# Kernel tuning notes

Hardware: AMD Instinct MI355X
Metric: run time of the kernel (lower is better)

## Reference

```python
import jax, jax.numpy as jnp
import numpy as np

DEPTH = 9
NUM_LEAVES = 2 ** DEPTH            # 512
NUM_BRANCHES = 2 ** DEPTH - 1      # 511


def _leaf_paths(depth):
    """For each leaf, the BFS (heap-order) branch indices along its root->leaf
    path and the left/right bit taken at each branch (1 = right)."""
    L = 2 ** depth
    idx = np.zeros((L, depth), np.int32)
    bits = np.zeros((L, depth), np.int32)
    for l in range(L):
        node = 0
        for t in range(depth):
            b = (l >> (depth - 1 - t)) & 1
            idx[l, t] = node
            bits[l, t] = b
            node = 2 * node + 1 + b
    return jnp.asarray(idx), jnp.asarray(bits)

PATH_IDX, PATH_BITS = _leaf_paths(DEPTH)


def setup_inputs() -> dict:
    key = jax.random.key(0)
    k1, k2, k3 = jax.random.split(key, 3)
    B, D, W, H = 128, 256, 28, 28
    C = 200
    return {
        "xs": jax.random.normal(k1, (B, D, W, H), jnp.float32),
        "prototypes": jax.random.normal(k2, (NUM_BRANCHES, D, 1, 1), jnp.float32),
        "leaf_params": jax.random.normal(k3, (NUM_LEAVES, C), jnp.float32),
    }


def reference(xs, prototypes, leaf_params):
    # ---- L2Conv2D: squared-L2 distance map via conv decomposition ----
    B, D, W, H = xs.shape
    P = prototypes.shape[0]
    p = prototypes.reshape(P, D)                       # W1 = H1 = 1
    x2 = jnp.sum(xs * xs, axis=1)                      # [B, W, H]
    p2 = jnp.sum(p * p, axis=1)                        # [P]
    xp = jnp.einsum('bdwh,pd->bpwh', xs, p)            # [B, P, W, H]
    sq = x2[:, None] - 2.0 * xp + p2[None, :, None, None]
    distances = jnp.sqrt(jnp.abs(sq) + 1e-14)          # [B, P, W, H]

    # ---- min-pool over full spatial extent (avg-pool unused: focal off) ----
    min_distances = jnp.min(distances, axis=(2, 3))    # [B, P]
    similarities = jnp.exp(-min_distances)             # [B, P], ps per branch

    # ---- soft tree routing: pa(leaf) = prod over path of ps / (1-ps) ----
    ps_path = similarities[:, PATH_IDX]                # [B, L, depth]
    step = jnp.where(PATH_BITS[None] == 1, ps_path, 1.0 - ps_path)
    pa = jnp.prod(step, axis=-1)                       # [B, L]

    # ---- mix leaf class distributions (distributed sampling strategy) ----
    ds = jax.nn.softmax(leaf_params, axis=-1)          # [L, C]
    return pa @ ds                                     # [B, C]
```

## Files before the change

### kernel.cpp

```cpp
#include <hip/hip_runtime.h>
#include <hip/hip_bf16.h>

typedef __attribute__((ext_vector_type(8))) int   i32x8;
typedef __attribute__((ext_vector_type(4))) int   i32x4;
typedef __attribute__((ext_vector_type(4))) float f32x4;

#define D_K    256
#define WH     784
#define WHH    392
#define P_REAL 511
#define P_PAD  512
#define C_OUT  200
#define NLEAF  512
#define TDEPTH 9

#define NT      32
#define NTILES  13
#define TILE_B  8192

#define WS_PB8  0
#define WS_P2   131072
#define WS_DS   133120
#define WS_PM   542720

#define SCALE_ONE 0x7F7F7F7F

__global__ __launch_bounds__(64)
void prep2_kernel(const float* __restrict__ protos, const float* __restrict__ lp,
                  unsigned char* __restrict__ pb8, float* __restrict__ p2,
                  float* __restrict__ ds) {
    int bid = blockIdx.x;
    int l = threadIdx.x;
    if (bid < P_PAD) {
        int p = bid;
        f32x4 v = {0.f, 0.f, 0.f, 0.f};
        if (p < P_REAL)
            v = *reinterpret_cast<const f32x4*>(protos + (size_t)p * D_K + 4 * l);
        int u = 0;
        u = __builtin_amdgcn_cvt_pk_fp8_f32(-2.f * v[0], -2.f * v[1], u, false);
        u = __builtin_amdgcn_cvt_pk_fp8_f32(-2.f * v[2], -2.f * v[3], u, true);
        *reinterpret_cast<int*>(pb8 + (size_t)p * D_K + 4 * l) = u;
        float s = v[0]*v[0] + v[1]*v[1] + v[2]*v[2] + v[3]*v[3];
#pragma unroll
        for (int m = 32; m >= 1; m >>= 1) s += __shfl_xor(s, m, 64);
        if (l == 0) p2[p] = s;
    } else {
        int row = bid - P_PAD;
        float v[4];
        float mx = -3.4e38f;
#pragma unroll
        for (int i = 0; i < 4; ++i) {
            int c = l + 64 * i;
            v[i] = (c < C_OUT) ? lp[(size_t)row * C_OUT + c] : -3.4e38f;
            mx = fmaxf(mx, v[i]);
        }
#pragma unroll
        for (int m = 32; m >= 1; m >>= 1) mx = fmaxf(mx, __shfl_xor(mx, m, 64));
        float sum = 0.f;
#pragma unroll
        for (int i = 0; i < 4; ++i) {
            int c = l + 64 * i;
            if (c < C_OUT) { v[i] = expf(v[i] - mx); sum += v[i]; }
        }
#pragma unroll
        for (int m = 32; m >= 1; m >>= 1) sum += __shfl_xor(sum, m, 64);
        float inv = 1.f / sum;
#pragma unroll
        for (int i = 0; i < 4; ++i) {
            int c = l + 64 * i;
            if (c < C_OUT) ds[(size_t)row * C_OUT + c] = v[i] * inv;
        }
    }
}

__global__ __launch_bounds__(512, 2)
void proto_min_kernel(const float* __restrict__ xs,
                      const unsigned char* __restrict__ pb8,
                      float* __restrict__ pm) {
    __shared__ unsigned char Xs[2][TILE_B];
    __shared__ float x2buf[2][8*68 + 8];

    const int tid  = threadIdx.x;
    const int wv   = tid >> 6;
    const int lane = tid & 63;
    const int lh   = lane >> 4;
    const int lr   = lane & 15;

    const int b   = blockIdx.x >> 1;
    const int whh = blockIdx.x & 1;

    const float* xb = xs + (size_t)b * (D_K * WH) + whh * WHH;

    i32x8 af[4][2];
#pragma unroll
    for (int mf = 0; mf < 4; ++mf) {
        const unsigned char* rp = pb8 + (size_t)(64*wv + 16*mf + lr) * D_K + lh*32;
        af[mf][0] = *reinterpret_cast<const i32x8*>(rp);
        af[mf][1] = *reinterpret_cast<const i32x8*>(rp + 128);
    }

    const int n4 = tid & 7;
    const int kq = tid >> 3;

    f32x4 rmin[4];
#pragma unroll
    for (int mf = 0; mf < 4; ++mf)
        rmin[mf] = (f32x4){3.0e38f, 3.0e38f, 3.0e38f, 3.0e38f};

    f32x4 ldA[4], ldB[4];

#define LOAD_T(T, LD) do {                                                    \
        int colb = (T) * NT + 4 * n4;                                         \
        if (colb > WHH - 4) colb = WHH - 4;                                   \
        const float* rowp = xb + (size_t)(4*kq) * WH + colb;                  \
        _Pragma("unroll")                                                     \
        for (int r = 0; r < 4; ++r)                                           \
            LD[r] = *reinterpret_cast<const f32x4*>(rowp + r * WH);           \
    } while (0)

#define STAGE_T(DST, LD) do {                                                 \
        f32x4 x2a = {0.f, 0.f, 0.f, 0.f};                                     \
        _Pragma("unroll")                                                     \
        for (int r = 0; r < 4; ++r) {                                         \
            f32x4 v = LD[r];                                                  \
            x2a[0] += v[0]*v[0]; x2a[1] += v[1]*v[1];                         \
            x2a[2] += v[2]*v[2]; x2a[3] += v[3]*v[3];                         \
        }                                                                     \
        _Pragma("unroll")                                                     \
        for (int c = 0; c < 4; ++c) {                                         \
            int n = 4*n4 + c;                                                 \
            int key = (n ^ (n >> 2)) & 7;                                     \
            int u = 0;                                                        \
            u = __builtin_amdgcn_cvt_pk_fp8_f32(LD[0][c], LD[1][c], u, false);\
            u = __builtin_amdgcn_cvt_pk_fp8_f32(LD[2][c], LD[3][c], u, true); \
            int off = n*256 + (((kq >> 2) ^ key) << 4) + ((kq & 3) << 2);     \
            *reinterpret_cast<int*>(&Xs[DST][off]) = u;                       \
        }                                                                     \
        _Pragma("unroll")                                                     \
        for (int c = 0; c < 4; ++c) {                                         \
            x2a[c] += __shfl_xor(x2a[c], 8, 64);                              \
            x2a[c] += __shfl_xor(x2a[c], 16, 64);                             \
            x2a[c] += __shfl_xor(x2a[c], 32, 64);                             \
        }                                                                     \
        if (lane < 8) {                                                       \
            _Pragma("unroll")                                                 \
            for (int c = 0; c < 4; ++c)                                       \
                x2buf[DST][lane*68 + c*8 + wv] = x2a[c];                      \
        }                                                                     \
    } while (0)

#define MFMA_TILE(CUR) do {                                                   \
        float x2v[2];                                                         \
        _Pragma("unroll")                                                     \
        for (int nf = 0; nf < 2; ++nf) {                                      \
            int n = 16*nf + lr;                                               \
            const float* xp = &x2buf[CUR][(n >> 2)*68 + (n & 3)*8];           \
            f32x4 q0 = *reinterpret_cast<const f32x4*>(xp);                   \
            f32x4 q1 = *reinterpret_cast<const f32x4*>(xp + 4);               \
            x2v[nf] = ((q0[0]+q0[1]) + (q0[2]+q0[3]))                         \
                    + ((q1[0]+q1[1]) + (q1[2]+q1[3]));                        \
        }                                                                     \
        f32x4 acc[4][2];                                                      \
        _Pragma("unroll")                                                     \
        for (int mf = 0; mf < 4; ++mf) {                                      \
            acc[mf][0] = (f32x4){x2v[0], x2v[0], x2v[0], x2v[0]};             \
            acc[mf][1] = (f32x4){x2v[1], x2v[1], x2v[1], x2v[1]};             \
        }                                                                     \
        __builtin_amdgcn_s_setprio(1);                                        \
        _Pragma("unroll")                                                     \
        for (int ks = 0; ks < 2; ++ks) {                                      \
            i32x8 bfr[2];                                                     \
            _Pragma("unroll")                                                 \
            for (int nf = 0; nf < 2; ++nf) {                                  \
                int n = 16*nf + lr;                                           \
                int key = (n ^ (n >> 2)) & 7;                                 \
                int kg0 = ks*8 + lh*2;                                        \
                i32x4 lo = *reinterpret_cast<const i32x4*>(                   \
                               &Xs[CUR][n*256 + ((kg0 ^ key) << 4)]);         \
                i32x4 hi = *reinterpret_cast<const i32x4*>(                   \
                               &Xs[CUR][n*256 + (((kg0 + 1) ^ key) << 4)]);   \
                bfr[nf] = __builtin_shufflevector(lo, hi, 0,1,2,3,4,5,6,7);   \
            }                                                                 \
            _Pragma("unroll")                                                 \
            for (int mf = 0; mf < 4; ++mf)                                    \
                _Pragma("unroll")                                             \
                for (int nf = 0; nf < 2; ++nf)                                \
                    acc[mf][nf] = __builtin_amdgcn_mfma_scale_f32_16x16x128_f8f6f4( \
                        af[mf][ks], bfr[nf], acc[mf][nf],                     \
                        0, 0, 0, SCALE_ONE, 0, SCALE_ONE);                    \
        }                                                                     \
        __builtin_amdgcn_s_setprio(0);                                        \
        _Pragma("unroll")                                                     \
        for (int mf = 0; mf < 4; ++mf)                                        \
            _Pragma("unroll")                                                 \
            for (int r = 0; r < 4; ++r)                                       \
                rmin[mf][r] = fminf(rmin[mf][r],                              \
                                    fminf(acc[mf][0][r], acc[mf][1][r]));     \
    } while (0)

#define TILE_BODY(T, CUR, NXT, LD) do {                                       \
        MFMA_TILE(CUR);                                                       \
        STAGE_T(NXT, LD);                                                     \
        if ((T) + 3 < NTILES) LOAD_T((T) + 3, LD);                            \
        __syncthreads();                                                      \
    } while (0)

    LOAD_T(0, ldA);
    STAGE_T(0, ldA);
    LOAD_T(1, ldA);
    LOAD_T(2, ldB);
    __syncthreads();

    for (int tt = 0; tt < 6; ++tt) {
        const int t0 = 2 * tt;
        TILE_BODY(t0,     0, 1, ldA);
        TILE_BODY(t0 + 1, 1, 0, ldB);
    }

    MFMA_TILE(0);

#pragma unroll
    for (int mf = 0; mf < 4; ++mf)
#pragma unroll
        for (int r = 0; r < 4; ++r) {
            float v = rmin[mf][r];
#pragma unroll
            for (int m = 1; m <= 8; m <<= 1)
                v = fminf(v, __shfl_xor(v, m, 64));
            rmin[mf][r] = v;
        }

    if (lr == 0) {
        float* pmw = pm + ((size_t)b * 2 + whh) * P_PAD;
#pragma unroll
        for (int mf = 0; mf < 4; ++mf)
#pragma unroll
            for (int r = 0; r < 4; ++r)
                pmw[64*wv + 16*mf + 4*lh + r] = rmin[mf][r];
    }
#undef LOAD_T
#undef STAGE_T
#undef MFMA_TILE
#undef TILE_BODY
}

__global__ __launch_bounds__(256)
void out_kernel(const float* __restrict__ pm, const float* __restrict__ p2,
                const float* __restrict__ ds, float* __restrict__ out) {
    __shared__ float sim[NLEAF];
    __shared__ float pa[NLEAF];
    int b = blockIdx.x;
    int t = threadIdx.x;
    const float* pm0 = pm + (size_t)b * 2 * P_PAD;
#pragma unroll
    for (int j = 0; j < 2; ++j) {
        int p = t + 256 * j;
        float m = fminf(pm0[p], pm0[P_PAD + p]);
        float sq = m + p2[p];
        sim[p] = expf(-sqrtf(fabsf(sq) + 1e-14f));
    }
    __syncthreads();
#pragma unroll
    for (int j = 0; j < 2; ++j) {
        int leaf = t + 256 * j;
        int node = 0;
        float prod = 1.f;
#pragma unroll
        for (int st = 0; st < TDEPTH; ++st) {
            int bit = (leaf >> (TDEPTH - 1 - st)) & 1;
            float sv = sim[node];
            prod *= bit ? sv : (1.f - sv);
            node = 2 * node + 1 + bit;
        }
        pa[leaf] = prod;
    }
    __syncthreads();
    if (t < C_OUT) {
        float a0 = 0.f, a1 = 0.f, a2 = 0.f, a3 = 0.f;
        for (int l = 0; l < NLEAF; l += 4) {
            a0 += pa[l + 0] * ds[(size_t)(l + 0) * C_OUT + t];
            a1 += pa[l + 1] * ds[(size_t)(l + 1) * C_OUT + t];
            a2 += pa[l + 2] * ds[(size_t)(l + 2) * C_OUT + t];
            a3 += pa[l + 3] * ds[(size_t)(l + 3) * C_OUT + t];
        }
        out[(size_t)b * C_OUT + t] = (a0 + a1) + (a2 + a3);
    }
}

extern "C" void kernel_launch(void* const* d_in, const int* in_sizes, int n_in,
                              void* d_out, int out_size, void* d_ws, size_t ws_size,
                              hipStream_t stream) {
    (void)in_sizes; (void)n_in; (void)out_size; (void)ws_size;
    const float* xs     = (const float*)d_in[0];
    const float* protos = (const float*)d_in[1];
    const float* lp     = (const float*)d_in[2];
    float* out = (float*)d_out;

    char* ws = (char*)d_ws;
    unsigned char* pb8 = (unsigned char*)(ws + WS_PB8);
    float* p2   = (float*)(ws + WS_P2);
    float* dsm  = (float*)(ws + WS_DS);
    float* pm   = (float*)(ws + WS_PM);

    prep2_kernel<<<1024, 64, 0, stream>>>(protos, lp, pb8, p2, dsm);
    proto_min_kernel<<<256, 512, 0, stream>>>(xs, pb8, pm);
    out_kernel<<<128, 256, 0, stream>>>(pm, p2, dsm, out);
}
```

Baseline: 49.99 us.

## Deepen LDS pipeline to four buffers and sync once per tile pair

Expands the shared-memory tile ring from two to four stages and processes tiles in pairs, issuing one barrier per pair instead of one per tile. The goal is to cut __syncthreads overhead and give global loads more time to land before they are staged. LDS use per block roughly doubles (about 32KB for the X tiles), which may limit the two-blocks-per-CU occupancy target, and register pressure from the extra in-flight loads could rise.

```diff
diff --git a/kernel.cpp b/kernel.cpp
--- a/kernel.cpp
+++ b/kernel.cpp
@@ -77,8 +77,8 @@
 void proto_min_kernel(const float* __restrict__ xs,
                       const unsigned char* __restrict__ pb8,
                       float* __restrict__ pm) {
-    __shared__ unsigned char Xs[2][TILE_B];
-    __shared__ float x2buf[2][8*68 + 8];
+    __shared__ unsigned char Xs[4][TILE_B];
+    __shared__ float x2buf[4][8*68 + 8];
 
     const int tid  = threadIdx.x;
     const int wv   = tid >> 6;
@@ -198,24 +198,30 @@
                                     fminf(acc[mf][0][r], acc[mf][1][r]));     \
     } while (0)
 
-#define TILE_BODY(T, CUR, NXT, LD) do {                                       \
-        MFMA_TILE(CUR);                                                       \
-        STAGE_T(NXT, LD);                                                     \
-        if ((T) + 3 < NTILES) LOAD_T((T) + 3, LD);                            \
+#define PAIR(T0, CA, CB, SA, SB) do {                                         \
+        MFMA_TILE(CA);                                                        \
+        STAGE_T(SA, ldA);                                                     \
+        if ((T0) + 4 < NTILES) LOAD_T((T0) + 4, ldA);                         \
+        MFMA_TILE(CB);                                                        \
+        if ((T0) + 3 < NTILES) {                                              \
+            STAGE_T(SB, ldB);                                                 \
+            if ((T0) + 5 < NTILES) LOAD_T((T0) + 5, ldB);                     \
+        }                                                                     \
         __syncthreads();                                                      \
     } while (0)
 
-    LOAD_T(0, ldA);
-    STAGE_T(0, ldA);
-    LOAD_T(1, ldA);
-    LOAD_T(2, ldB);
+    LOAD_T(0, ldA); STAGE_T(0, ldA);
+    LOAD_T(1, ldA); STAGE_T(1, ldA);
+    LOAD_T(2, ldA);
+    LOAD_T(3, ldB);
     __syncthreads();
 
-    for (int tt = 0; tt < 6; ++tt) {
-        const int t0 = 2 * tt;
-        TILE_BODY(t0,     0, 1, ldA);
-        TILE_BODY(t0 + 1, 1, 0, ldB);
-    }
+    PAIR(0,  0, 1, 2, 3);
+    PAIR(2,  2, 3, 0, 1);
+    PAIR(4,  0, 1, 2, 3);
+    PAIR(6,  2, 3, 0, 1);
+    PAIR(8,  0, 1, 2, 3);
+    PAIR(10, 2, 3, 0, 1);
 
     MFMA_TILE(0);
 
@@ -241,7 +247,7 @@
 #undef LOAD_T
 #undef STAGE_T
 #undef MFMA_TILE
-#undef TILE_BODY
+#undef PAIR
 }
 
 __global__ __launch_bounds__(256)
```

Measured after the change: 85.65 us. +71.3%, slower.

## Split proto_min_kernel into producer and consumer waves

Applied to the files above, without the earlier changes.

The block size grows from 512 to 1024 threads, and the waves are specialised by role. Waves 0-7 keep the fp8 prototype fragments in registers and only run the MFMA/min loop. Waves 8-15 only load xs tiles from global memory, convert them to fp8 and stage them into double-buffered LDS with x2 sums. The goal is to let global loads and conversion overlap fully with MFMA work, instead of interleaving them in the same waves, and to double the resident waves per CU. The risks are that each role carries its own barrier count, which must stay matched, and that one 1024-thread block per CU limits the registers each wave can use.

```diff
diff --git a/kernel.cpp b/kernel.cpp
--- a/kernel.cpp
+++ b/kernel.cpp
@@ -73,7 +73,7 @@
     }
 }
 
-__global__ __launch_bounds__(512, 2)
+__global__ __launch_bounds__(1024, 1)
 void proto_min_kernel(const float* __restrict__ xs,
                       const unsigned char* __restrict__ pb8,
                       float* __restrict__ pm) {
@@ -83,31 +83,11 @@
     const int tid  = threadIdx.x;
     const int wv   = tid >> 6;
     const int lane = tid & 63;
-    const int lh   = lane >> 4;
-    const int lr   = lane & 15;
 
     const int b   = blockIdx.x >> 1;
     const int whh = blockIdx.x & 1;
 
     const float* xb = xs + (size_t)b * (D_K * WH) + whh * WHH;
-
-    i32x8 af[4][2];
-#pragma unroll
-    for (int mf = 0; mf < 4; ++mf) {
-        const unsigned char* rp = pb8 + (size_t)(64*wv + 16*mf + lr) * D_K + lh*32;
-        af[mf][0] = *reinterpret_cast<const i32x8*>(rp);
-        af[mf][1] = *reinterpret_cast<const i32x8*>(rp + 128);
-    }
-
-    const int n4 = tid & 7;
-    const int kq = tid >> 3;
-
-    f32x4 rmin[4];
-#pragma unroll
-    for (int mf = 0; mf < 4; ++mf)
-        rmin[mf] = (f32x4){3.0e38f, 3.0e38f, 3.0e38f, 3.0e38f};
-
-    f32x4 ldA[4], ldB[4];
 
 #define LOAD_T(T, LD) do {                                                    \
         int colb = (T) * NT + 4 * n4;                                         \
@@ -145,7 +125,7 @@
         if (lane < 8) {                                                       \
             _Pragma("unroll")                                                 \
             for (int c = 0; c < 4; ++c)                                       \
-                x2buf[DST][lane*68 + c*8 + wv] = x2a[c];                      \
+                x2buf[DST][lane*68 + c*8 + (wv & 7)] = x2a[c];                \
         }                                                                     \
     } while (0)
 
@@ -198,50 +178,75 @@
                                     fminf(acc[mf][0][r], acc[mf][1][r]));     \
     } while (0)
 
-#define TILE_BODY(T, CUR, NXT, LD) do {                                       \
-        MFMA_TILE(CUR);                                                       \
-        STAGE_T(NXT, LD);                                                     \
-        if ((T) + 3 < NTILES) LOAD_T((T) + 3, LD);                            \
-        __syncthreads();                                                      \
-    } while (0)
-
-    LOAD_T(0, ldA);
-    STAGE_T(0, ldA);
-    LOAD_T(1, ldA);
-    LOAD_T(2, ldB);
-    __syncthreads();
-
-    for (int tt = 0; tt < 6; ++tt) {
-        const int t0 = 2 * tt;
-        TILE_BODY(t0,     0, 1, ldA);
-        TILE_BODY(t0 + 1, 1, 0, ldB);
-    }
-
-    MFMA_TILE(0);
-
-#pragma unroll
-    for (int mf = 0; mf < 4; ++mf)
-#pragma unroll
-        for (int r = 0; r < 4; ++r) {
-            float v = rmin[mf][r];
-#pragma unroll
-            for (int m = 1; m <= 8; m <<= 1)
-                v = fminf(v, __shfl_xor(v, m, 64));
-            rmin[mf][r] = v;
-        }
-
-    if (lr == 0) {
-        float* pmw = pm + ((size_t)b * 2 + whh) * P_PAD;
+    if (wv < 8) {
+        const int lh = lane >> 4;
+        const int lr = lane & 15;
+
+        i32x8 af[4][2];
+#pragma unroll
+        for (int mf = 0; mf < 4; ++mf) {
+            const unsigned char* rp = pb8 + (size_t)(64*wv + 16*mf + lr) * D_K + lh*32;
+            af[mf][0] = *reinterpret_cast<const i32x8*>(rp);
+            af[mf][1] = *reinterpret_cast<const i32x8*>(rp + 128);
+        }
+
+        f32x4 rmin[4];
 #pragma unroll
         for (int mf = 0; mf < 4; ++mf)
-#pragma unroll
-            for (int r = 0; r < 4; ++r)
-                pmw[64*wv + 16*mf + 4*lh + r] = rmin[mf][r];
+            rmin[mf] = (f32x4){3.0e38f, 3.0e38f, 3.0e38f, 3.0e38f};
+
+        __syncthreads();
+        for (int t = 0; t < NTILES; ++t) {
+            MFMA_TILE(t & 1);
+            __syncthreads();
+        }
+
+#pragma unroll
+        for (int mf = 0; mf < 4; ++mf)
+#pragma unroll
+            for (int r = 0; r < 4; ++r) {
+                float v = rmin[mf][r];
+#pragma unroll
+                for (int m = 1; m <= 8; m <<= 1)
+                    v = fminf(v, __shfl_xor(v, m, 64));
+                rmin[mf][r] = v;
+            }
+
+        if (lr == 0) {
+            float* pmw = pm + ((size_t)b * 2 + whh) * P_PAD;
+#pragma unroll
+            for (int mf = 0; mf < 4; ++mf)
+#pragma unroll
+                for (int r = 0; r < 4; ++r)
+                    pmw[64*wv + 16*mf + 4*lh + r] = rmin[mf][r];
+        }
+    } else {
+        const int pid = tid - 512;
+        const int n4  = pid & 7;
+        const int kq  = pid >> 3;
+
+        f32x4 ldA[4], ldB[4];
+
+        LOAD_T(0, ldA);
+        STAGE_T(0, ldA);
+        LOAD_T(1, ldA);
+        LOAD_T(2, ldB);
+        __syncthreads();
+
+        for (int tt = 0; tt < 6; ++tt) {
+            const int t0 = 2 * tt;
+            STAGE_T(1, ldA);
+            if (t0 + 3 < NTILES) LOAD_T(t0 + 3, ldA);
+            __syncthreads();
+            STAGE_T(0, ldB);
+            if (t0 + 4 < NTILES) LOAD_T(t0 + 4, ldB);
+            __syncthreads();
+        }
+        __syncthreads();
     }
 #undef LOAD_T
 #undef STAGE_T
 #undef MFMA_TILE
-#undef TILE_BODY
 }
 
 __global__ __launch_bounds__(256)
@@ -303,6 +308,6 @@
     float* pm   = (float*)(ws + WS_PM);
 
     prep2_kernel<<<1024, 64, 0, stream>>>(protos, lp, pb8, p2, dsm);
-    proto_min_kernel<<<256, 512, 0, stream>>>(xs, pb8, pm);
+    proto_min_kernel<<<256, 1024, 0, stream>>>(xs, pb8, pm);
     out_kernel<<<128, 256, 0, stream>>>(pm, p2, dsm, out);
 }
```

After: 70.97 us. 1.42x slower.
